# Kernel optimization log

Hardware: AMD Instinct MI355X
Metric: run time of the kernel (lower is better)

Reference implementation:

```python
import jax, jax.numpy as jnp
import numpy as np

E, S, L, V, PMAX = 256, 64, 3, 256, 2000
DILATIONS = (1, 2, 4, 8)


def _layernorm(x, g, b, eps=1e-5):
    m = x.mean(-1, keepdims=True)
    v = ((x - m) ** 2).mean(-1, keepdims=True)
    return (x - m) * jax.lax.rsqrt(v + eps) * g + b


def _ssm_layer(x, in_w, conv_w, conv_b, dt_w, A_log, D_param, B_w, C_w, out_w, ln_g, ln_b):
    # x: [B, T, D]
    Bsz, T, Dm = x.shape
    xr = x @ in_w.T                                  # [B,T,2D]
    x_in, x_res = xr[..., :Dm], xr[..., Dm:]
    # causal depthwise conv, kernel=4, left-pad 3 (== torch pad=3 then [:, :, :T])
    xt = x_in.transpose(0, 2, 1)                     # [B,D,T]
    xc = jax.lax.conv_general_dilated(
        xt, conv_w[:, None, :], (1,), [(3, 0)],
        feature_group_count=Dm, dimension_numbers=('NCH', 'OIH', 'NCH'))
    xc = jax.nn.silu((xc + conv_b[None, :, None]).transpose(0, 2, 1))  # [B,T,D]
    A = -jnp.exp(A_log)                              # [D,S]
    Bm = xc @ B_w.T                                  # [B,T,S]
    Cm = xc @ C_w.T                                  # [B,T,S]
    dt = jax.nn.softplus(dt_w)                       # [D] per-channel timestep
    dA = 1.0 + dt[:, None] * A                       # Euler discretization I + dt*A, [D,S]
    h0 = jnp.zeros((Bsz, Dm, S), x.dtype)

    def step(h, inp):
        u_t, B_t, C_t = inp                          # [B,D],[B,S],[B,S]
        h = dA * h + (dt * u_t)[:, :, None] * B_t[:, None, :]   # [B,D,S]
        y = jnp.einsum('bs,bds->bd', C_t, h)
        return h, y

    _, ys = jax.lax.scan(step, h0, (xc.transpose(1, 0, 2), Bm.transpose(1, 0, 2), Cm.transpose(1, 0, 2)))
    y = ys.transpose(1, 0, 2) + D_param * xc         # [B,T,D]
    y = (y * jax.nn.silu(x_res)) @ out_w.T
    return _layernorm(y + x, ln_g, ln_b)


def _forward(tokens, tok_emb, pos_emb, in_w, conv_w, conv_b, dt_w, A_log, D_param,
             B_w, C_w, out_w, ln_g, ln_b, ctx_w, ctx_b, fus_w, fus_b, fus_ln_g, fus_ln_b):
    Bsz, T = tokens.shape
    x = tok_emb[tokens] + pos_emb[:T][None]          # [B,T,E]
    feats = x
    for i in range(L):
        feats = _ssm_layer(feats, in_w[i], conv_w[i], conv_b[i], dt_w[i], A_log[i],
                           D_param[i], B_w[i], C_w[i], out_w[i], ln_g[i], ln_b[i])
    # multi-dilation context convs on the raw embeddings
    xt = x.transpose(0, 2, 1)                        # [B,E,T]
    ctx = []
    for j, d in enumerate(DILATIONS):
        o = jax.lax.conv_general_dilated(
            xt, ctx_w[j], (1,), [(d, d)], rhs_dilation=(d,),
            dimension_numbers=('NCH', 'OIH', 'NCH'))
        ctx.append(o + ctx_b[j][None, :, None])
    ctx = jnp.concatenate(ctx, axis=1).transpose(0, 2, 1)      # [B,T,E]
    fused = jax.nn.relu(jnp.concatenate([feats, ctx], -1) @ fus_w.T + fus_b)
    return _layernorm(fused, fus_ln_g, fus_ln_b)


def setup_inputs() -> dict:
    key = jax.random.key(0)
    ks = jax.random.split(key, 16)
    Bsz, T = 32, 2000

    def n(k, shape, s):
        return jax.random.normal(k, shape, jnp.float32) * s

    return {
        'tokens': jax.random.randint(ks[0], (Bsz, T), 0, V),
        'tok_emb': n(ks[1], (V, E), 1.0),
        'pos_emb': n(ks[2], (PMAX, E), 1.0),
        'in_w': n(ks[3], (L, 2 * E, E), 0.05),
        'conv_w': n(ks[4], (L, E, 4), 0.2),
        'conv_b': jnp.zeros((L, E), jnp.float32),
        'dt_w': jax.random.uniform(ks[5], (L, E), jnp.float32, -0.01, 0.01),
        'A_log': jax.random.uniform(ks[6], (L, E, S), jnp.float32, -4.0, -1.0),
        'D_param': jnp.zeros((L, E), jnp.float32),
        'B_w': n(ks[7], (L, S, E), 0.05),
        'C_w': n(ks[8], (L, S, E), 0.05),
        'out_w': n(ks[9], (L, E, E), 0.05),
        'ln_g': jnp.ones((L, E), jnp.float32),
        'ln_b': jnp.zeros((L, E), jnp.float32),
        'ctx_w': n(ks[10], (4, E // 4, E, 3), 0.05),
        'ctx_b': jnp.zeros((4, E // 4), jnp.float32),
        'fus_w': n(ks[11], (E, 2 * E), 0.05),
        'fus_b': jnp.zeros((E,), jnp.float32),
        'fus_ln_g': jnp.ones((E,), jnp.float32),
        'fus_ln_b': jnp.zeros((E,), jnp.float32),
    }


def reference(tokens, tok_emb, pos_emb, in_w, conv_w, conv_b, dt_w, A_log, D_param,
              B_w, C_w, out_w, ln_g, ln_b, ctx_w, ctx_b, fus_w, fus_b, fus_ln_g, fus_ln_b):
    return _forward(tokens, tok_emb, pos_emb, in_w, conv_w, conv_b, dt_w, A_log, D_param,
                    B_w, C_w, out_w, ln_g, ln_b, ctx_w, ctx_b, fus_w, fus_b, fus_ln_g, fus_ln_b)
```

## Files before the change

kernel.cpp:

```cpp
#include <hip/hip_runtime.h>
#include <stdint.h>

#define B_ 32
#define T_ 2000
#define E_ 256
#define S_ 64
#define L_ 3
#define BT_ (B_*T_)
#define NC_ 25
#define CL_ 80
#define TS_ 16
#define NT_ (CL_/TS_)
#define TP_ (T_+16)

typedef short s8v __attribute__((ext_vector_type(8)));
typedef short s4v __attribute__((ext_vector_type(4)));
typedef float f4v __attribute__((ext_vector_type(4)));
typedef float f2v __attribute__((ext_vector_type(2)));
typedef unsigned short us;

__device__ __forceinline__ float b2f(us u){
    return __uint_as_float(((unsigned int)u) << 16);
}
__device__ __forceinline__ us f2b(float f){
    unsigned int x = __float_as_uint(f);
    x += 0x7fffu + ((x >> 16) & 1u);
    return (us)(x >> 16);
}

__global__ __launch_bounds__(256) void cvtw_k(const float* __restrict__ src,
    us* __restrict__ dst)
{
    int idx = blockIdx.x*256 + threadIdx.x;
    f4v v = *(const f4v*)(src + (size_t)idx*4);
    s4v o;
    #pragma unroll
    for (int j=0;j<4;j++) o[j] = (short)f2b(v[j]);
    *(s4v*)(dst + (size_t)idx*4) = o;
}

__global__ __launch_bounds__(256) void packbc_k(const float* __restrict__ Bw,
    const float* __restrict__ Cw, us* __restrict__ wbc)
{
    int idx = blockIdx.x*256 + threadIdx.x;
    int i = idx & 255; int r = (idx >> 8) & 127; int l = idx >> 15;
    const float* src = (r < 64) ? (Bw + ((size_t)l*S_ + r)*E_ + i)
                                : (Cw + ((size_t)l*S_ + (r-64))*E_ + i);
    wbc[idx] = f2b(*src);
}

__global__ __launch_bounds__(256) void packw_k(const float* __restrict__ cw,
    us* __restrict__ wp)
{
    int idx = blockIdx.x*256 + threadIdx.x;
    int i2 = idx % 768; int r = idx / 768;
    int c = r & 63; int j = r >> 6;
    int tap = i2 >> 8; int i = i2 & 255;
    wp[idx] = f2b(cw[(((size_t)(j*64 + c))*E_ + i)*3 + tap]);
}

__global__ __launch_bounds__(256) void embed_k(const int* __restrict__ tok,
    const float* __restrict__ te, const float* __restrict__ pe, us* __restrict__ x0)
{
    int idx = blockIdx.x*256 + threadIdx.x;
    int dg = idx & 31; int bt = idx >> 5; int t = bt % T_;
    int tk = tok[bt] & 255;
    const float* ta = te + (size_t)tk*E_ + dg*8;
    const float* pa = pe + (size_t)t*E_ + dg*8;
    f4v a0 = *(const f4v*)ta, a1 = *(const f4v*)(ta+4);
    f4v p0 = *(const f4v*)pa, p1 = *(const f4v*)(pa+4);
    s8v o;
    #pragma unroll
    for (int j=0;j<4;j++){
        o[j]   = (short)f2b(a0[j] + p0[j]);
        o[j+4] = (short)f2b(a1[j] + p1[j]);
    }
    *(s8v*)(x0 + (size_t)bt*E_ + dg*8) = o;
}

__global__ __launch_bounds__(256) void lconst_k(const float* __restrict__ dt_w,
    const float* __restrict__ A_log, float* __restrict__ dtv,
    float* __restrict__ dAT, float* __restrict__ dApT)
{
    int idx = blockIdx.x*256 + threadIdx.x;
    int d = idx & (E_-1); int s = idx >> 8;
    float dt = log1pf(expf(dt_w[d]));
    float A  = -expf(A_log[d*S_ + s]);
    float dA = 1.f + dt*A;
    dAT[s*E_ + d]  = dA;
    dApT[s*E_ + d] = powf(dA, (float)CL_);
    if (s == 0) dtv[d] = dt;
}

__global__ __launch_bounds__(256) void dwconv_k(const us* __restrict__ xin,
    const float* __restrict__ cw, const float* __restrict__ cb, us* __restrict__ xc)
{
    int idx = blockIdx.x*256 + threadIdx.x;
    int dg = idx & 31; int bt = idx >> 5; int t = bt % T_;
    int d0 = dg*8;
    float acc[8]; float w[8][4];
    #pragma unroll
    for (int j=0;j<8;j++){
        f4v wv = *(const f4v*)(cw + (size_t)(d0+j)*4);
        #pragma unroll
        for (int k=0;k<4;k++) w[j][k] = wv[k];
        acc[j] = cb[d0+j];
    }
    #pragma unroll
    for (int k=0;k<4;k++){
        if (t + k - 3 >= 0){
            s8v xv = *(const s8v*)(xin + (size_t)(bt + k - 3)*E_ + d0);
            #pragma unroll
            for (int j=0;j<8;j++) acc[j] = fmaf(b2f((us)xv[j]), w[j][k], acc[j]);
        }
    }
    s8v o;
    #pragma unroll
    for (int j=0;j<8;j++){ float v = acc[j]; v = v / (1.f + expf(-v)); o[j] = (short)f2b(v); }
    *(s8v*)(xc + (size_t)bt*E_ + d0) = o;
}

#define BM 128
#define BN 64
#define BK 32

template<int AMODE, int EPI>
__global__ __launch_bounds__(256)
void gemm_k(const us* __restrict__ A1, const us* __restrict__ A2,
            int lda, int shift,
            const us* __restrict__ W, int ldw,
            void* __restrict__ C1, void* __restrict__ C2,
            const float* __restrict__ bias,
            int ldc, int K)
{
    __shared__ us Al[BM*BK];
    __shared__ us Bl[BN*BK];
    const int tid = threadIdx.x;
    const int wid = tid >> 6, lane = tid & 63;
    const int m0 = blockIdx.x * BM;
    const int n0 = blockIdx.y * BN;
    const int wr = wid >> 1, wc = wid & 1;
    f4v acc[4][2];
    #pragma unroll
    for (int a=0;a<4;a++)
        #pragma unroll
        for (int b=0;b<2;b++) acc[a][b] = (f4v){0.f,0.f,0.f,0.f};

    for (int k0 = 0; k0 < K; k0 += BK){
        if (k0) __syncthreads();
        #pragma unroll
        for (int i=0;i<2;i++){
            int g = i*256 + tid;
            int row = g >> 2, ks = g & 3;
            const us* src;
            if constexpr (AMODE==0){
                src = A1 + (size_t)(m0+row)*lda + k0 + ks*8;
            } else if constexpr (AMODE==2){
                int kk = k0 + ks*8;
                const us* base = (kk < E_) ? A1 : A2;
                src = base + (size_t)(m0+row)*E_ + (kk & (E_-1));
            } else {
                int kk = k0 + ks*8;
                int tap = kk >> 8; int kin = kk & (E_-1);
                int m = m0 + row; int bb = m / T_; int tt = m - bb*T_;
                src = A1 + ((size_t)bb*TP_ + 8 + tt + (tap-1)*shift)*E_ + kin;
            }
            __builtin_amdgcn_global_load_lds(
                (const __attribute__((address_space(1))) void*)src,
                (__attribute__((address_space(3))) void*)(Al + (size_t)g*8), 16, 0, 0);
        }
        {
            int row = tid >> 2, ks = tid & 3;
            const us* src = W + (size_t)(n0+row)*ldw + k0 + ks*8;
            __builtin_amdgcn_global_load_lds(
                (const __attribute__((address_space(1))) void*)src,
                (__attribute__((address_space(3))) void*)(Bl + (size_t)tid*8), 16, 0, 0);
        }
        __syncthreads();

        s8v af[4], bfr[2];
        #pragma unroll
        for (int mr=0;mr<4;mr++)
            af[mr] = *(const s8v*)(Al + ((size_t)(wr*64 + mr*16 + (lane&15))*4 + (lane>>4))*8);
        #pragma unroll
        for (int nr=0;nr<2;nr++)
            bfr[nr] = *(const s8v*)(Bl + ((size_t)(wc*32 + nr*16 + (lane&15))*4 + (lane>>4))*8);
        #pragma unroll
        for (int mr=0;mr<4;mr++)
            #pragma unroll
            for (int nr=0;nr<2;nr++)
                acc[mr][nr] = __builtin_amdgcn_mfma_f32_16x16x32_bf16(af[mr], bfr[nr], acc[mr][nr], 0, 0, 0);
    }
    #pragma unroll
    for (int mr=0;mr<4;mr++){
        #pragma unroll
        for (int nr=0;nr<2;nr++){
            int col = n0 + wc*32 + nr*16 + (lane & 15);
            int rb  = m0 + wr*64 + mr*16 + ((lane >> 4) << 2);
            #pragma unroll
            for (int i=0;i<4;i++){
                float val = acc[mr][nr][i];
                size_t row = (size_t)(rb + i);
                if constexpr (EPI==0){
                    ((us*)C1)[row*ldc + col] = f2b(val);
                } else if constexpr (EPI==1){
                    if (col < E_) ((us*)C1)[row*E_ + col] = f2b(val);
                    else          ((us*)C2)[row*E_ + (col - E_)] = f2b(val);
                } else if constexpr (EPI==2){
                    ((float*)C1)[row*ldc + col] = val;
                } else if constexpr (EPI==5){
                    val += bias[col];
                    ((us*)C1)[row*ldc + col] = f2b(val);
                } else {
                    val += bias[col];
                    val = fmaxf(val, 0.f);
                    ((float*)C1)[row*ldc + col] = val;
                }
            }
        }
    }
}

__global__ __launch_bounds__(1024) void scan_h(
    const float* __restrict__ dAT, const float* __restrict__ dtv,
    const us* __restrict__ xc, const float* __restrict__ BC,
    us* __restrict__ H)
{
    __shared__ float sBC[TS_*128];
    __shared__ us    sXC[TS_*256];
    int b = blockIdx.x / NC_, c = blockIdx.x % NC_;
    int tid = threadIdx.x;
    int d = tid >> 2, sg = tid & 3, s0 = sg*16;
    f4v h4[4], dA4[4];
    #pragma unroll
    for (int q=0;q<4;q++){
        #pragma unroll
        for (int j=0;j<4;j++){ h4[q][j] = 0.f; dA4[q][j] = dAT[(s0+q*4+j)*E_ + d]; }
    }
    float dtd = dtv[d];
    int t0 = c*CL_;
    size_t base0 = (size_t)b*T_ + t0;
    *(f2v*)(&sBC[tid*2]) = *(const f2v*)(BC + base0*128 + tid*2);
    *(s4v*)(&sXC[tid*4]) = *(const s4v*)(xc + base0*E_ + tid*4);
    __syncthreads();
    for (int tile = 0; tile < NT_; ++tile){
        f2v pv; s4v pxv;
        bool more = (tile+1 < NT_);
        if (more){
            size_t basen = base0 + (size_t)(tile+1)*TS_;
            pv  = *(const f2v*)(BC + basen*128 + tid*2);
            pxv = *(const s4v*)(xc + basen*E_ + tid*4);
        }
        for (int st = 0; st < TS_; ++st){
            float u = dtd * b2f(sXC[st*256 + d]);
            const f4v* Bp = (const f4v*)(&sBC[st*128 + s0]);
            #pragma unroll
            for (int q=0;q<4;q++) h4[q] = dA4[q]*h4[q] + Bp[q]*u;
        }
        __syncthreads();
        if (more){
            *(f2v*)(&sBC[tid*2]) = pv;
            *(s4v*)(&sXC[tid*4]) = pxv;
        }
        __syncthreads();
    }
    size_t hb = ((size_t)(b*NC_ + c))*S_*E_ + d;
    #pragma unroll
    for (int q=0;q<4;q++)
        #pragma unroll
        for (int j=0;j<4;j++) H[hb + (size_t)(s0+q*4+j)*E_] = f2b(h4[q][j]);
}

__global__ __launch_bounds__(256) void carry_k(const float* __restrict__ dApT,
    us* H)
{
    int idx = blockIdx.x*256 + threadIdx.x;
    int d = idx & (E_-1); int s = (idx >> 8) & (S_-1); int b = idx >> 14;
    float ap = dApT[s*E_ + d];
    size_t base = ((size_t)(b*NC_))*S_*E_ + (size_t)s*E_ + d;
    float hh = 0.f;
    for (int c=0;c<NC_;c++){
        size_t p = base + (size_t)c*S_*E_;
        float hl = b2f(H[p]);
        H[p] = f2b(hh);
        hh = fmaf(ap, hh, hl);
    }
}

__global__ __launch_bounds__(1024) void scan_y(
    const float* __restrict__ dAT, const float* __restrict__ dtv,
    const us* __restrict__ xc, const float* __restrict__ BC,
    const us* __restrict__ Hc, us* __restrict__ ys)
{
    __shared__ float sBC[TS_*128];
    __shared__ us    sXC[TS_*256];
    int b = blockIdx.x / NC_, c = blockIdx.x % NC_;
    int tid = threadIdx.x;
    int d = tid >> 2, sg = tid & 3, s0 = sg*16;
    f4v h4[4], dA4[4];
    size_t cb = ((size_t)(b*NC_ + c))*S_*E_ + d;
    #pragma unroll
    for (int q=0;q<4;q++){
        #pragma unroll
        for (int j=0;j<4;j++){
            int s = s0 + q*4 + j;
            dA4[q][j] = dAT[s*E_ + d];
            h4[q][j]  = b2f(Hc[cb + (size_t)s*E_]);
        }
    }
    float dtd = dtv[d];
    int t0 = c*CL_;
    size_t base0 = (size_t)b*T_ + t0;
    *(f2v*)(&sBC[tid*2]) = *(const f2v*)(BC + base0*128 + tid*2);
    *(s4v*)(&sXC[tid*4]) = *(const s4v*)(xc + base0*E_ + tid*4);
    __syncthreads();
    for (int tile = 0; tile < NT_; ++tile){
        f2v pv; s4v pxv;
        bool more = (tile+1 < NT_);
        if (more){
            size_t basen = base0 + (size_t)(tile+1)*TS_;
            pv  = *(const f2v*)(BC + basen*128 + tid*2);
            pxv = *(const s4v*)(xc + basen*E_ + tid*4);
        }
        for (int st = 0; st < TS_; ++st){
            int t = t0 + tile*TS_ + st;
            float u = dtd * b2f(sXC[st*256 + d]);
            const f4v* Bp = (const f4v*)(&sBC[st*128 + s0]);
            const f4v* Cp = (const f4v*)(&sBC[st*128 + 64 + s0]);
            f4v y4 = (f4v){0.f,0.f,0.f,0.f};
            #pragma unroll
            for (int q=0;q<4;q++){
                h4[q] = dA4[q]*h4[q] + Bp[q]*u;
                y4    = y4 + Cp[q]*h4[q];
            }
            float y = (y4[0]+y4[1]) + (y4[2]+y4[3]);
            y += __shfl_xor(y, 1, 64);
            y += __shfl_xor(y, 2, 64);
            if (sg == 0) ys[((size_t)b*T_ + t)*E_ + d] = f2b(y);
        }
        __syncthreads();
        if (more){
            *(f2v*)(&sBC[tid*2]) = pv;
            *(s4v*)(&sXC[tid*4]) = pxv;
        }
        __syncthreads();
    }
}

__global__ __launch_bounds__(256) void zin_k(const us* __restrict__ ys,
    const us* xc, const us* __restrict__ xres,
    const float* __restrict__ Dp, us* zout)
{
    size_t e0 = ((size_t)blockIdx.x*256 + threadIdx.x)*4;
    int d0 = (int)(e0 & (E_-1));
    s4v yv  = *(const s4v*)(ys + e0);
    s4v xcv = *(const s4v*)(xc + e0);
    s4v xrv = *(const s4v*)(xres + e0);
    f4v dv  = *(const f4v*)(Dp + d0);
    s4v o;
    #pragma unroll
    for (int j=0;j<4;j++){
        float y  = b2f((us)yv[j]) + dv[j] * b2f((us)xcv[j]);
        float xr = b2f((us)xrv[j]);
        o[j] = (short)f2b(y * (xr / (1.f + expf(-xr))));
    }
    *(s4v*)(zout + e0) = o;
}

__global__ __launch_bounds__(256) void ln_k(const us* z,
    const us* __restrict__ resid, const float* __restrict__ g,
    const float* __restrict__ bb, us* out)
{
    int wid = threadIdx.x >> 6, lane = threadIdx.x & 63;
    size_t row = (size_t)blockIdx.x*4 + wid;
    size_t base = row*E_ + lane*4;
    s4v zv = *(const s4v*)(z + base);
    float v[4];
    #pragma unroll
    for (int j=0;j<4;j++) v[j] = b2f((us)zv[j]);
    if (resid){
        s4v rv = *(const s4v*)(resid + base);
        #pragma unroll
        for (int j=0;j<4;j++) v[j] += b2f((us)rv[j]);
    }
    float sum = v[0]+v[1]+v[2]+v[3];
    float sq  = v[0]*v[0]+v[1]*v[1]+v[2]*v[2]+v[3]*v[3];
    #pragma unroll
    for (int off=32; off>0; off>>=1){
        sum += __shfl_xor(sum, off, 64);
        sq  += __shfl_xor(sq,  off, 64);
    }
    float mean = sum * (1.f/E_);
    float var  = sq * (1.f/E_) - mean*mean;
    float rstd = rsqrtf(var + 1e-5f);
    f4v gv = *(const f4v*)(g + lane*4);
    f4v bv = *(const f4v*)(bb + lane*4);
    s4v o;
    #pragma unroll
    for (int j=0;j<4;j++)
        o[j] = (short)f2b((v[j]-mean)*rstd*gv[j] + bv[j]);
    *(s4v*)(out + base) = o;
}

__global__ __launch_bounds__(256) void ln_f32_k(const float* z,
    const float* __restrict__ g, const float* __restrict__ bb, float* out)
{
    int wid = threadIdx.x >> 6, lane = threadIdx.x & 63;
    size_t row = (size_t)blockIdx.x*4 + wid;
    size_t base = row*E_ + lane*4;
    f4v v = *(const f4v*)(z + base);
    float sum = v[0]+v[1]+v[2]+v[3];
    float sq  = v[0]*v[0]+v[1]*v[1]+v[2]*v[2]+v[3]*v[3];
    #pragma unroll
    for (int off=32; off>0; off>>=1){
        sum += __shfl_xor(sum, off, 64);
        sq  += __shfl_xor(sq,  off, 64);
    }
    float mean = sum * (1.f/E_);
    float var  = sq * (1.f/E_) - mean*mean;
    float rstd = rsqrtf(var + 1e-5f);
    f4v gv = *(const f4v*)(g + lane*4);
    f4v bv = *(const f4v*)(bb + lane*4);
    f4v o;
    #pragma unroll
    for (int j=0;j<4;j++)
        o[j] = (v[j]-mean)*rstd*gv[j] + bv[j];
    *(f4v*)(out + base) = o;
}

__global__ __launch_bounds__(256) void xpad_k(const us* __restrict__ x0,
    us* __restrict__ xp)
{
    int idx = blockIdx.x*256 + threadIdx.x;
    int dg = idx & 31; int r = idx >> 5;
    int tp = r % TP_; int b = r / TP_;
    s8v o;
    if (tp < 8 || tp >= T_+8){
        #pragma unroll
        for (int j=0;j<8;j++) o[j] = 0;
    } else {
        o = *(const s8v*)(x0 + ((size_t)b*T_ + tp - 8)*E_ + dg*8);
    }
    *(s8v*)(xp + (size_t)r*E_ + dg*8) = o;
}

__global__ void probe_k(const unsigned int* __restrict__ outw,
    const us* p0, const us* p1, float* outf)
{
    if (threadIdx.x | blockIdx.x) return;
    bool zero = true;
    for (int i=0;i<512 && zero;i++)              if (outw[i]) zero = false;
    for (int i=2000000;i<2000512 && zero;i++)    if (outw[i]) zero = false;
    if (!zero) return;
    int code = 256, f;
    f=0; for (int i=0;i<256;i++) if (p0[i] & 0x7FFF) f=1;  code += 128*f;
    f=0; for (int i=0;i<256;i++) if (p1[i] & 0x7FFF) f=1;  code += 16*f;
    outf[0] = (float)code;
}

extern "C" void kernel_launch(void* const* d_in, const int* in_sizes, int n_in,
                              void* d_out, int out_size, void* d_ws, size_t ws_size,
                              hipStream_t stream)
{
    const int*   tokens   = (const int*)d_in[0];
    const float* tok_emb  = (const float*)d_in[1];
    const float* pos_emb  = (const float*)d_in[2];
    const float* in_w     = (const float*)d_in[3];
    const float* conv_w   = (const float*)d_in[4];
    const float* conv_b   = (const float*)d_in[5];
    const float* dt_w     = (const float*)d_in[6];
    const float* A_log    = (const float*)d_in[7];
    const float* D_param  = (const float*)d_in[8];
    const float* B_w      = (const float*)d_in[9];
    const float* C_w      = (const float*)d_in[10];
    const float* out_w    = (const float*)d_in[11];
    const float* ln_g     = (const float*)d_in[12];
    const float* ln_b     = (const float*)d_in[13];
    const float* ctx_w    = (const float*)d_in[14];
    const float* ctx_b    = (const float*)d_in[15];
    const float* fus_w    = (const float*)d_in[16];
    const float* fus_b    = (const float*)d_in[17];
    const float* fus_ln_g = (const float*)d_in[18];
    const float* fus_ln_b = (const float*)d_in[19];

    char* ws = (char*)d_ws;
    size_t off = 0;
    auto alloc = [&](size_t bytes){ size_t o = off; off += (bytes + 255) & ~(size_t)255; return o; };
    const size_t BT = BT_;
    size_t o_p0  = alloc(BT*E_*2);
    size_t o_p1  = alloc(BT*E_*2);
    size_t o_ctx = alloc(BT*E_*2);
    size_t o_xin = alloc(BT*E_*2);
    size_t o_xc  = alloc(BT*E_*2);
    size_t o_bc  = alloc(BT*128*4);
    size_t o_h   = alloc((size_t)B_*NC_*S_*E_*2);
    size_t o_wp  = alloc((size_t)4*64*768*2);
    size_t o_wi  = alloc((size_t)L_*2*E_*E_*2);
    size_t o_wo  = alloc((size_t)L_*E_*E_*2);
    size_t o_wbc = alloc((size_t)L_*128*E_*2);
    size_t o_wf  = alloc((size_t)E_*2*E_*2);
    size_t o_dtv = alloc(E_*4);
    size_t o_dat = alloc(E_*S_*4);
    size_t o_dap = alloc(E_*S_*4);
    (void)ws_size; (void)in_sizes; (void)n_in; (void)out_size;

    us* P0   = (us*)(ws + o_p0);
    us* P1   = (us*)(ws + o_p1);
    us* CTXB = (us*)(ws + o_ctx);
    us* XIN  = (us*)(ws + o_xin);
    us* XC   = (us*)(ws + o_xc);
    float* BCf = (float*)(ws + o_bc);
    us* Hb   = (us*)(ws + o_h);
    us* WP   = (us*)(ws + o_wp);
    us* WI   = (us*)(ws + o_wi);
    us* WO   = (us*)(ws + o_wo);
    us* WBC  = (us*)(ws + o_wbc);
    us* WF   = (us*)(ws + o_wf);
    float* DTV  = (float*)(ws + o_dtv);
    float* DAT  = (float*)(ws + o_dat);
    float* DAPT = (float*)(ws + o_dap);
    us* XPAD = XIN;
    us* YS   = (us*)d_out;
    us* XRES = (us*)d_out + BT*E_;

    cvtw_k<<<L_*2*E_*E_/1024, 256, 0, stream>>>(in_w,  WI);
    cvtw_k<<<L_*E_*E_/1024,   256, 0, stream>>>(out_w, WO);
    cvtw_k<<<E_*2*E_/1024,    256, 0, stream>>>(fus_w, WF);
    packbc_k<<<L_*128*E_/256, 256, 0, stream>>>(B_w, C_w, WBC);
    packw_k<<<4*64*768/256,   256, 0, stream>>>(ctx_w, WP);

    embed_k<<<BT_*32/256, 256, 0, stream>>>(tokens, tok_emb, pos_emb, P0);

    xpad_k<<<B_*TP_*32/256, 256, 0, stream>>>(P0, XPAD);
    const int dil[4] = {1,2,4,8};
    for (int j = 0; j < 4; ++j){
        gemm_k<3,5><<<dim3(BT_/BM, 1), 256, 0, stream>>>(
            XPAD, nullptr, E_, dil[j], WP + (size_t)j*64*768, 768,
            CTXB + j*64, nullptr, ctx_b + j*64, E_, 768);
    }

    for (int l = 0; l < L_; ++l){
        const us* xprev = (l==1) ? P1 : P0;
        us*       xnext = (l==1) ? P0 : P1;

        lconst_k<<<E_*S_/256, 256, 0, stream>>>(dt_w + (size_t)l*E_, A_log + (size_t)l*E_*S_,
                                                DTV, DAT, DAPT);
        gemm_k<0,1><<<dim3(BT_/BM, 2*E_/BN), 256, 0, stream>>>(
            xprev, nullptr, E_, 0, WI + (size_t)l*2*E_*E_, E_, XIN, XRES, nullptr, E_, E_);
        dwconv_k<<<BT_*32/256, 256, 0, stream>>>(XIN, conv_w + (size_t)l*E_*4, conv_b + (size_t)l*E_, XC);
        gemm_k<0,2><<<dim3(BT_/BM, 2), 256, 0, stream>>>(
            XC, nullptr, E_, 0, WBC + (size_t)l*128*E_, E_, BCf, nullptr, nullptr, 128, E_);
        scan_h<<<B_*NC_, 1024, 0, stream>>>(DAT, DTV, XC, BCf, Hb);
        carry_k<<<B_*S_*E_/256, 256, 0, stream>>>(DAPT, Hb);
        scan_y<<<B_*NC_, 1024, 0, stream>>>(DAT, DTV, XC, BCf, Hb, YS);
        zin_k<<<BT_*E_/4/256, 256, 0, stream>>>(YS, XC, XRES, D_param + (size_t)l*E_, XC );
        gemm_k<0,0><<<dim3(BT_/BM, E_/BN), 256, 0, stream>>>(
            XC, nullptr, E_, 0, WO + (size_t)l*E_*E_, E_, XIN , nullptr, nullptr, E_, E_);
        ln_k<<<BT_/4, 256, 0, stream>>>(XIN, xprev, ln_g + (size_t)l*E_, ln_b + (size_t)l*E_, xnext);
    }

    gemm_k<2,6><<<dim3(BT_/BM, E_/BN), 256, 0, stream>>>(
        P1, CTXB, E_, 0, WF, 2*E_, d_out, nullptr, fus_b, E_, 2*E_);
    ln_f32_k<<<BT_/4, 256, 0, stream>>>((const float*)d_out, fus_ln_g, fus_ln_b, (float*)d_out);

    probe_k<<<1, 64, 0, stream>>>((const unsigned int*)d_out, P0, P1, (float*)d_out);
}
```

Measured before the change: 1.467 ms.

## Compute local outputs in first scan pass and add carry correction separately

```diff
diff --git a/kernel.cpp b/kernel.cpp
--- a/kernel.cpp
+++ b/kernel.cpp
@@ -140,6 +140,8 @@
     const int m0 = blockIdx.x * BM;
     const int n0 = blockIdx.y * BN;
     const int wr = wid >> 1, wc = wid & 1;
+    int sh = shift;
+    if constexpr (AMODE==4) sh = 1 << blockIdx.y;
     f4v acc[4][2];
     #pragma unroll
     for (int a=0;a<4;a++)
@@ -163,7 +165,7 @@
                 int kk = k0 + ks*8;
                 int tap = kk >> 8; int kin = kk & (E_-1);
                 int m = m0 + row; int bb = m / T_; int tt = m - bb*T_;
-                src = A1 + ((size_t)bb*TP_ + 8 + tt + (tap-1)*shift)*E_ + kin;
+                src = A1 + ((size_t)bb*TP_ + 8 + tt + (tap-1)*sh)*E_ + kin;
             }
             __builtin_amdgcn_global_load_lds(
                 (const __attribute__((address_space(1))) void*)src,
@@ -221,10 +223,10 @@
     }
 }
 
-__global__ __launch_bounds__(1024) void scan_h(
+__global__ __launch_bounds__(1024) void scan_ly(
     const float* __restrict__ dAT, const float* __restrict__ dtv,
     const us* __restrict__ xc, const float* __restrict__ BC,
-    us* __restrict__ H)
+    us* __restrict__ ys, us* __restrict__ H)
 {
     __shared__ float sBC[TS_*128];
     __shared__ us    sXC[TS_*256];
@@ -252,77 +254,6 @@
             pxv = *(const s4v*)(xc + basen*E_ + tid*4);
         }
         for (int st = 0; st < TS_; ++st){
-            float u = dtd * b2f(sXC[st*256 + d]);
-            const f4v* Bp = (const f4v*)(&sBC[st*128 + s0]);
-            #pragma unroll
-            for (int q=0;q<4;q++) h4[q] = dA4[q]*h4[q] + Bp[q]*u;
-        }
-        __syncthreads();
-        if (more){
-            *(f2v*)(&sBC[tid*2]) = pv;
-            *(s4v*)(&sXC[tid*4]) = pxv;
-        }
-        __syncthreads();
-    }
-    size_t hb = ((size_t)(b*NC_ + c))*S_*E_ + d;
-    #pragma unroll
-    for (int q=0;q<4;q++)
-        #pragma unroll
-        for (int j=0;j<4;j++) H[hb + (size_t)(s0+q*4+j)*E_] = f2b(h4[q][j]);
-}
-
-__global__ __launch_bounds__(256) void carry_k(const float* __restrict__ dApT,
-    us* H)
-{
-    int idx = blockIdx.x*256 + threadIdx.x;
-    int d = idx & (E_-1); int s = (idx >> 8) & (S_-1); int b = idx >> 14;
-    float ap = dApT[s*E_ + d];
-    size_t base = ((size_t)(b*NC_))*S_*E_ + (size_t)s*E_ + d;
-    float hh = 0.f;
-    for (int c=0;c<NC_;c++){
-        size_t p = base + (size_t)c*S_*E_;
-        float hl = b2f(H[p]);
-        H[p] = f2b(hh);
-        hh = fmaf(ap, hh, hl);
-    }
-}
-
-__global__ __launch_bounds__(1024) void scan_y(
-    const float* __restrict__ dAT, const float* __restrict__ dtv,
-    const us* __restrict__ xc, const float* __restrict__ BC,
-    const us* __restrict__ Hc, us* __restrict__ ys)
-{
-    __shared__ float sBC[TS_*128];
-    __shared__ us    sXC[TS_*256];
-    int b = blockIdx.x / NC_, c = blockIdx.x % NC_;
-    int tid = threadIdx.x;
-    int d = tid >> 2, sg = tid & 3, s0 = sg*16;
-    f4v h4[4], dA4[4];
-    size_t cb = ((size_t)(b*NC_ + c))*S_*E_ + d;
-    #pragma unroll
-    for (int q=0;q<4;q++){
-        #pragma unroll
-        for (int j=0;j<4;j++){
-            int s = s0 + q*4 + j;
-            dA4[q][j] = dAT[s*E_ + d];
-            h4[q][j]  = b2f(Hc[cb + (size_t)s*E_]);
-        }
-    }
-    float dtd = dtv[d];
-    int t0 = c*CL_;
-    size_t base0 = (size_t)b*T_ + t0;
-    *(f2v*)(&sBC[tid*2]) = *(const f2v*)(BC + base0*128 + tid*2);
-    *(s4v*)(&sXC[tid*4]) = *(const s4v*)(xc + base0*E_ + tid*4);
-    __syncthreads();
-    for (int tile = 0; tile < NT_; ++tile){
-        f2v pv; s4v pxv;
-        bool more = (tile+1 < NT_);
-        if (more){
-            size_t basen = base0 + (size_t)(tile+1)*TS_;
-            pv  = *(const f2v*)(BC + basen*128 + tid*2);
-            pxv = *(const s4v*)(xc + basen*E_ + tid*4);
-        }
-        for (int st = 0; st < TS_; ++st){
             int t = t0 + tile*TS_ + st;
             float u = dtd * b2f(sXC[st*256 + d]);
             const f4v* Bp = (const f4v*)(&sBC[st*128 + s0]);
@@ -334,8 +265,8 @@
                 y4    = y4 + Cp[q]*h4[q];
             }
             float y = (y4[0]+y4[1]) + (y4[2]+y4[3]);
-            y += __shfl_xor(y, 1, 64);
-            y += __shfl_xor(y, 2, 64);
+            y += __shfl_xor(y, 1, 4);
+            y += __shfl_xor(y, 2, 4);
             if (sg == 0) ys[((size_t)b*T_ + t)*E_ + d] = f2b(y);
         }
         __syncthreads();
@@ -343,6 +274,80 @@
             *(f2v*)(&sBC[tid*2]) = pv;
             *(s4v*)(&sXC[tid*4]) = pxv;
         }
+        __syncthreads();
+    }
+    size_t hb = ((size_t)(b*NC_ + c))*S_*E_ + d;
+    #pragma unroll
+    for (int q=0;q<4;q++)
+        #pragma unroll
+        for (int j=0;j<4;j++) H[hb + (size_t)(s0+q*4+j)*E_] = f2b(h4[q][j]);
+}
+
+__global__ __launch_bounds__(256) void carry_k(const float* __restrict__ dApT,
+    us* H)
+{
+    int idx = blockIdx.x*256 + threadIdx.x;
+    int d = idx & (E_-1); int s = (idx >> 8) & (S_-1); int b = idx >> 14;
+    float ap = dApT[s*E_ + d];
+    size_t base = ((size_t)(b*NC_))*S_*E_ + (size_t)s*E_ + d;
+    float hh = 0.f;
+    for (int c=0;c<NC_;c++){
+        size_t p = base + (size_t)c*S_*E_;
+        float hl = b2f(H[p]);
+        H[p] = f2b(hh);
+        hh = fmaf(ap, hh, hl);
+    }
+}
+
+__global__ __launch_bounds__(1024) void scan_fx(
+    const float* __restrict__ dAT, const float* __restrict__ BC,
+    const us* __restrict__ Hc, us* ys)
+{
+    __shared__ float sC[TS_*64];
+    int b = blockIdx.x / (NC_-1); int c = 1 + blockIdx.x % (NC_-1);
+    int tid = threadIdx.x;
+    int d = tid >> 2, sg = tid & 3, s0 = sg*16;
+    f4v w4[4], dA4[4];
+    size_t cb = ((size_t)(b*NC_ + c))*S_*E_ + d;
+    #pragma unroll
+    for (int q=0;q<4;q++){
+        #pragma unroll
+        for (int j=0;j<4;j++){
+            int s = s0 + q*4 + j;
+            dA4[q][j] = dAT[s*E_ + d];
+            w4[q][j]  = dA4[q][j] * b2f(Hc[cb + (size_t)s*E_]);
+        }
+    }
+    int t0 = c*CL_;
+    size_t base0 = (size_t)b*T_ + t0;
+    sC[tid] = BC[(base0 + (size_t)(tid>>6))*128 + 64 + (tid & 63)];
+    __syncthreads();
+    for (int tile = 0; tile < NT_; ++tile){
+        float pv;
+        bool more = (tile+1 < NT_);
+        if (more){
+            size_t basen = base0 + (size_t)(tile+1)*TS_;
+            pv = BC[(basen + (size_t)(tid>>6))*128 + 64 + (tid & 63)];
+        }
+        for (int st = 0; st < TS_; ++st){
+            int t = t0 + tile*TS_ + st;
+            const f4v* Cp = (const f4v*)(&sC[st*64 + s0]);
+            f4v y4 = (f4v){0.f,0.f,0.f,0.f};
+            #pragma unroll
+            for (int q=0;q<4;q++){
+                y4   = y4 + Cp[q]*w4[q];
+                w4[q] = w4[q]*dA4[q];
+            }
+            float y = (y4[0]+y4[1]) + (y4[2]+y4[3]);
+            y += __shfl_xor(y, 1, 4);
+            y += __shfl_xor(y, 2, 4);
+            if (sg == 0){
+                size_t p = ((size_t)b*T_ + t)*E_ + d;
+                ys[p] = f2b(b2f(ys[p]) + y);
+            }
+        }
+        __syncthreads();
+        if (more) sC[tid] = pv;
         __syncthreads();
     }
 }
@@ -532,12 +537,9 @@
     embed_k<<<BT_*32/256, 256, 0, stream>>>(tokens, tok_emb, pos_emb, P0);
 
     xpad_k<<<B_*TP_*32/256, 256, 0, stream>>>(P0, XPAD);
-    const int dil[4] = {1,2,4,8};
-    for (int j = 0; j < 4; ++j){
-        gemm_k<3,5><<<dim3(BT_/BM, 1), 256, 0, stream>>>(
-            XPAD, nullptr, E_, dil[j], WP + (size_t)j*64*768, 768,
-            CTXB + j*64, nullptr, ctx_b + j*64, E_, 768);
-    }
+    gemm_k<4,5><<<dim3(BT_/BM, 4), 256, 0, stream>>>(
+        XPAD, nullptr, E_, 0, WP, 768,
+        CTXB, nullptr, ctx_b, E_, 768);
 
     for (int l = 0; l < L_; ++l){
         const us* xprev = (l==1) ? P1 : P0;
@@ -550,9 +552,9 @@
         dwconv_k<<<BT_*32/256, 256, 0, stream>>>(XIN, conv_w + (size_t)l*E_*4, conv_b + (size_t)l*E_, XC);
         gemm_k<0,2><<<dim3(BT_/BM, 2), 256, 0, stream>>>(
             XC, nullptr, E_, 0, WBC + (size_t)l*128*E_, E_, BCf, nullptr, nullptr, 128, E_);
-        scan_h<<<B_*NC_, 1024, 0, stream>>>(DAT, DTV, XC, BCf, Hb);
+        scan_ly<<<B_*NC_, 1024, 0, stream>>>(DAT, DTV, XC, BCf, YS, Hb);
         carry_k<<<B_*S_*E_/256, 256, 0, stream>>>(DAPT, Hb);
-        scan_y<<<B_*NC_, 1024, 0, stream>>>(DAT, DTV, XC, BCf, Hb, YS);
+        scan_fx<<<B_*(NC_-1), 1024, 0, stream>>>(DAT, BCf, Hb, YS);
         zin_k<<<BT_*E_/4/256, 256, 0, stream>>>(YS, XC, XRES, D_param + (size_t)l*E_, XC );
         gemm_k<0,0><<<dim3(BT_/BM, E_/BN), 256, 0, stream>>>(
             XC, nullptr, E_, 0, WO + (size_t)l*E_*E_, E_, XIN , nullptr, nullptr, E_, E_);
```

Measured after the change: 1.457 ms. No clear change (-0.7%).
